# Kernel tuning notes

Measured on AMD Instinct MI355X. Metric: run time of the kernel, lower is better.

Reference implementation:

```python
import jax, jax.numpy as jnp
import numpy as np

N = 100000  # number of nodes
E = 3200000  # number of edges (avg degree 32)


def spmm(rows, cols, vals, Y):
    # sparse A (COO) @ dense Y : gather rows of Y at cols, scale, scatter-add to rows
    return jax.ops.segment_sum(vals[:, None] * Y[cols], rows, num_segments=N)


def setup_inputs() -> dict:
    key = jax.random.key(0)
    kx, kr, kc, kv, k0, k1 = jax.random.split(key, 6)
    X = jax.random.normal(kx, (N, 512), dtype=jnp.float32)
    edge_rows = jax.random.randint(kr, (E,), 0, N, dtype=jnp.int32)
    edge_cols = jax.random.randint(kc, (E,), 0, N, dtype=jnp.int32)
    edge_vals = jax.random.uniform(kv, (E,), dtype=jnp.float32)
    W0 = jax.random.normal(k0, (512, 256), dtype=jnp.float32) * 0.05
    W1 = jax.random.normal(k1, (256, 64), dtype=jnp.float32) * 0.05
    return {"X": X, "edge_rows": edge_rows, "edge_cols": edge_cols,
            "edge_vals": edge_vals, "W0": W0, "W1": W1}


def reference(X, edge_rows, edge_cols, edge_vals, W0, W1):
    # layer 1: A_hat @ (X W0), relu
    H1 = jax.nn.relu(spmm(edge_rows, edge_cols, edge_vals, X @ W0))  # [N, H]
    # layer 2: A_hat @ (H1 W1), softmax over classes
    Z = spmm(edge_rows, edge_cols, edge_vals, H1 @ W1)  # [N, F]
    return jax.nn.softmax(Z, axis=-1)
```

## Files before the change

### kernel.cpp

```cpp
#include <hip/hip_runtime.h>
#include <hip/hip_bf16.h>
#include <hip/hip_fp16.h>
#include <cstdint>

#define N_NODES 100000
#define N_EDGES 3200000
#define F_IN    512
#define F_HID   256
#define F_OUT   64
#define CAP     96

typedef _Float16 half8_t __attribute__((ext_vector_type(8)));
typedef _Float16 half4_t __attribute__((ext_vector_type(4)));
typedef float    float4_t __attribute__((ext_vector_type(4)));


__global__ __launch_bounds__(256) void zero_cursors_kernel(int* __restrict__ cursor, int n) {
    int i = blockIdx.x * 256 + threadIdx.x;
    if (i < n) cursor[i] = 0;
}

__global__ __launch_bounds__(256) void ell_scatter_kernel(
    const int* __restrict__ rows, const int* __restrict__ cols,
    const float* __restrict__ vals, int* __restrict__ cursor,
    int* __restrict__ ell_col, float* __restrict__ ell_val, int e_count) {
    int e = blockIdx.x * 256 + threadIdx.x;
    if (e >= e_count) return;
    int r = rows[e];
    int p = atomicAdd(&cursor[r], 1);
    if (p < CAP) {
        ell_col[(size_t)r * CAP + p] = cols[e];
        ell_val[(size_t)r * CAP + p] = vals[e];
    }
}


__global__ __launch_bounds__(256) void convert_w_kernel(
    const float* __restrict__ W0, const float* __restrict__ W1,
    _Float16* __restrict__ W0T, _Float16* __restrict__ W1T) {
    int i = blockIdx.x * 256 + threadIdx.x;
    if (i < F_HID * F_IN) {
        int n = i >> 9, k = i & 511;
        W0T[i] = (_Float16)W0[k * F_HID + n];
    }
    int j = i - F_HID * F_IN;
    if (j >= 0 && j < F_OUT * F_HID) {
        int n = j >> 8, k = j & 255;
        W1T[j] = (_Float16)W1[k * F_OUT + n];
    }
}


__global__ __launch_bounds__(256) void gemm1_mfma_kernel(
    const float* __restrict__ X, const _Float16* __restrict__ W0T,
    _Float16* __restrict__ H0) {
    const int wave = threadIdx.x >> 6;
    const int lane = threadIdx.x & 63;
    const int l15  = lane & 15;
    const int quad = lane >> 4;
    const int m0   = blockIdx.x * 64;
    const int n0   = wave * 64;

    float4_t acc[4][4] = {};

    int row[4];
    #pragma unroll
    for (int mt = 0; mt < 4; mt++) {
        int r = m0 + mt * 16 + l15;
        row[mt] = r < N_NODES ? r : N_NODES - 1;
    }

    for (int k0 = 0; k0 < F_IN; k0 += 32) {
        const int kk = k0 + quad * 8;
        half8_t b[4];
        #pragma unroll
        for (int nt = 0; nt < 4; nt++)
            b[nt] = *(const half8_t*)(W0T + (size_t)(n0 + nt * 16 + l15) * F_IN + kk);

        half8_t a[4];
        #pragma unroll
        for (int mt = 0; mt < 4; mt++) {
            const float* p = X + (size_t)row[mt] * F_IN + kk;
            float4_t lo = *(const float4_t*)p;
            float4_t hi = *(const float4_t*)(p + 4);
            half8_t f;
            f[0] = (_Float16)lo[0]; f[1] = (_Float16)lo[1];
            f[2] = (_Float16)lo[2]; f[3] = (_Float16)lo[3];
            f[4] = (_Float16)hi[0]; f[5] = (_Float16)hi[1];
            f[6] = (_Float16)hi[2]; f[7] = (_Float16)hi[3];
            a[mt] = f;
        }

        #pragma unroll
        for (int mt = 0; mt < 4; mt++)
            #pragma unroll
            for (int nt = 0; nt < 4; nt++)
                acc[mt][nt] = __builtin_amdgcn_mfma_f32_16x16x32_f16(
                    a[mt], b[nt], acc[mt][nt], 0, 0, 0);
    }

    #pragma unroll
    for (int mt = 0; mt < 4; mt++)
        #pragma unroll
        for (int reg = 0; reg < 4; reg++) {
            int m = m0 + mt * 16 + quad * 4 + reg;
            if (m < N_NODES) {
                #pragma unroll
                for (int nt = 0; nt < 4; nt++)
                    H0[(size_t)m * F_HID + n0 + nt * 16 + l15] =
                        (_Float16)acc[mt][nt][reg];
            }
        }
}


__global__ __launch_bounds__(256) void gemm2_mfma_kernel(
    const _Float16* __restrict__ H1, const _Float16* __restrict__ W1T,
    _Float16* __restrict__ H2) {
    const int wave = threadIdx.x >> 6;
    const int lane = threadIdx.x & 63;
    const int l15  = lane & 15;
    const int quad = lane >> 4;
    const int m0   = blockIdx.x * 64 + wave * 16;

    int r = m0 + l15;
    if (r >= N_NODES) r = N_NODES - 1;

    float4_t acc[4] = {};

    for (int k0 = 0; k0 < F_HID; k0 += 32) {
        const int kk = k0 + quad * 8;
        half8_t a = *(const half8_t*)(H1 + (size_t)r * F_HID + kk);
        #pragma unroll
        for (int nt = 0; nt < 4; nt++) {
            half8_t b = *(const half8_t*)(W1T + (size_t)(nt * 16 + l15) * F_HID + kk);
            acc[nt] = __builtin_amdgcn_mfma_f32_16x16x32_f16(a, b, acc[nt], 0, 0, 0);
        }
    }

    #pragma unroll
    for (int reg = 0; reg < 4; reg++) {
        int m = m0 + quad * 4 + reg;
        if (m < N_NODES) {
            #pragma unroll
            for (int nt = 0; nt < 4; nt++)
                H2[(size_t)m * F_OUT + nt * 16 + l15] = (_Float16)acc[nt][reg];
        }
    }
}


__global__ __launch_bounds__(256) void spmm_relu_kernel(
    const _Float16* __restrict__ H0, const int* __restrict__ ell_col,
    const float* __restrict__ ell_val, const int* __restrict__ cursor,
    _Float16* __restrict__ H1) {
    const int r = blockIdx.x * 4 + (threadIdx.x >> 6);
    const int t = threadIdx.x & 63;
    int n = cursor[r]; if (n > CAP) n = CAP;
    const int*   cols = ell_col + (size_t)r * CAP;
    const float* vals = ell_val + (size_t)r * CAP;
    const half4_t* H0v = (const half4_t*)H0;

    float4_t acc = {};
    int j = 0;
    for (; j + 4 <= n; j += 4) {
        int4   c = *(const int4*)(cols + j);
        float4 v = *(const float4*)(vals + j);
        half4_t g0 = H0v[(size_t)c.x * 64 + t];
        half4_t g1 = H0v[(size_t)c.y * 64 + t];
        half4_t g2 = H0v[(size_t)c.z * 64 + t];
        half4_t g3 = H0v[(size_t)c.w * 64 + t];
        #pragma unroll
        for (int i = 0; i < 4; i++) {
            acc[i] = fmaf(v.x, (float)g0[i], acc[i]);
            acc[i] = fmaf(v.y, (float)g1[i], acc[i]);
            acc[i] = fmaf(v.z, (float)g2[i], acc[i]);
            acc[i] = fmaf(v.w, (float)g3[i], acc[i]);
        }
    }
    for (; j < n; j++) {
        half4_t g = H0v[(size_t)cols[j] * 64 + t];
        float vv = vals[j];
        #pragma unroll
        for (int i = 0; i < 4; i++) acc[i] = fmaf(vv, (float)g[i], acc[i]);
    }
    half4_t o;
    #pragma unroll
    for (int i = 0; i < 4; i++) o[i] = (_Float16)fmaxf(acc[i], 0.f);
    ((half4_t*)H1)[(size_t)r * 64 + t] = o;
}


__global__ __launch_bounds__(256) void spmm_softmax_kernel(
    const _Float16* __restrict__ H2, const int* __restrict__ ell_col,
    const float* __restrict__ ell_val, const int* __restrict__ cursor,
    float* __restrict__ out) {
    const int lane = threadIdx.x & 63;
    const int r = blockIdx.x * 4 + (threadIdx.x >> 6);
    int n = cursor[r]; if (n > CAP) n = CAP;
    const int*   cols = ell_col + (size_t)r * CAP;
    const float* vals = ell_val + (size_t)r * CAP;
    float acc = 0.f;
    int j = 0;
    for (; j + 4 <= n; j += 4) {
        int4   c = *(const int4*)(cols + j);
        float4 v = *(const float4*)(vals + j);
        acc = fmaf(v.x, (float)H2[(size_t)c.x * F_OUT + lane], acc);
        acc = fmaf(v.y, (float)H2[(size_t)c.y * F_OUT + lane], acc);
        acc = fmaf(v.z, (float)H2[(size_t)c.z * F_OUT + lane], acc);
        acc = fmaf(v.w, (float)H2[(size_t)c.w * F_OUT + lane], acc);
    }
    for (; j < n; j++)
        acc = fmaf(vals[j], (float)H2[(size_t)cols[j] * F_OUT + lane], acc);

    float m = acc;
    #pragma unroll
    for (int o = 32; o >= 1; o >>= 1) m = fmaxf(m, __shfl_xor(m, o, 64));
    float e = expf(acc - m);
    float s = e;
    #pragma unroll
    for (int o = 32; o >= 1; o >>= 1) s += __shfl_xor(s, o, 64);
    out[(size_t)r * F_OUT + lane] = e / s;
}


extern "C" void kernel_launch(void* const* d_in, const int* in_sizes, int n_in,
                              void* d_out, int out_size, void* d_ws, size_t ws_size,
                              hipStream_t stream) {
    const float* X     = (const float*)d_in[0];
    const int*   erows = (const int*)  d_in[1];
    const int*   ecols = (const int*)  d_in[2];
    const float* evals = (const float*)d_in[3];
    const float* W0    = (const float*)d_in[4];
    const float* W1    = (const float*)d_in[5];
    float* out = (float*)d_out;

    char* p = (char*)d_ws;
    _Float16* H0  = (_Float16*)p; p += (size_t)N_NODES * F_HID * 2;
    _Float16* H1  = (_Float16*)p; p += (size_t)N_NODES * F_HID * 2;
    _Float16* H2  = (_Float16*)p; p += (size_t)N_NODES * F_OUT * 2;
    _Float16* W0T = (_Float16*)p; p += (size_t)F_HID * F_IN * 2;
    _Float16* W1T = (_Float16*)p; p += (size_t)F_OUT * F_HID * 2;
    int*   cursor  = (int*)p;     p += (size_t)N_NODES * 4;
    int*   ell_col = (int*)p;     p += (size_t)N_NODES * CAP * 4;
    float* ell_val = (float*)p;

    zero_cursors_kernel<<<(N_NODES + 255) / 256, 256, 0, stream>>>(cursor, N_NODES);
    ell_scatter_kernel<<<(N_EDGES + 255) / 256, 256, 0, stream>>>(
        erows, ecols, evals, cursor, ell_col, ell_val, N_EDGES);
    convert_w_kernel<<<(F_HID * F_IN + F_OUT * F_HID + 255) / 256, 256, 0, stream>>>(
        W0, W1, W0T, W1T);

    gemm1_mfma_kernel<<<(N_NODES + 63) / 64, 256, 0, stream>>>(X, W0T, H0);

    spmm_relu_kernel<<<N_NODES / 4, 256, 0, stream>>>(H0, ell_col, ell_val, cursor, H1);

    gemm2_mfma_kernel<<<(N_NODES + 63) / 64, 256, 0, stream>>>(H1, W1T, H2);

    spmm_softmax_kernel<<<N_NODES / 4, 256, 0, stream>>>(H2, ell_col, ell_val, cursor, out);
}
```

Baseline: 989.7 us.

## Interleave ELL col/val, pad cursors, retile GEMM1, widen SpMM gathers

Packs ELL column and value into one uint2 array so each edge is a single 8-byte load. Pads the per-row atomic cursors to a 16-int stride to spread atomic contention. GEMM1 uses a pre-swizzled W0 fragment layout and a 2x2 wave tiling (32 rows by 128 columns per wave), so the X rows each wave reloads and converts are halved and B loads are contiguous. Both SpMM kernels now split each wave into two half-waves that process alternate edges with wider 16-byte or 4-byte gathers, then combine via a shuffle. The padded cursor array adds zeroing traffic and the per-wave GEMM1 B loads double.

```diff
diff --git a/kernel.cpp b/kernel.cpp
--- a/kernel.cpp
+++ b/kernel.cpp
@@ -9,9 +9,10 @@
 #define F_HID   256
 #define F_OUT   64
 #define CAP     96
-
-typedef _Float16 half8_t __attribute__((ext_vector_type(8)));
-typedef _Float16 half4_t __attribute__((ext_vector_type(4)));
+#define CSTRIDE 16
+
+typedef _Float16 half8_t  __attribute__((ext_vector_type(8)));
+typedef _Float16 half2_t  __attribute__((ext_vector_type(2)));
 typedef float    float4_t __attribute__((ext_vector_type(4)));
 
 
@@ -23,25 +24,30 @@
 __global__ __launch_bounds__(256) void ell_scatter_kernel(
     const int* __restrict__ rows, const int* __restrict__ cols,
     const float* __restrict__ vals, int* __restrict__ cursor,
-    int* __restrict__ ell_col, float* __restrict__ ell_val, int e_count) {
+    uint2* __restrict__ ell, int e_count) {
     int e = blockIdx.x * 256 + threadIdx.x;
     if (e >= e_count) return;
     int r = rows[e];
-    int p = atomicAdd(&cursor[r], 1);
+    int p = atomicAdd(&cursor[r * CSTRIDE], 1);
     if (p < CAP) {
-        ell_col[(size_t)r * CAP + p] = cols[e];
-        ell_val[(size_t)r * CAP + p] = vals[e];
+        ell[(size_t)r * CAP + p] = make_uint2((unsigned)cols[e], __float_as_uint(vals[e]));
     }
 }
 
 
 __global__ __launch_bounds__(256) void convert_w_kernel(
     const float* __restrict__ W0, const float* __restrict__ W1,
-    _Float16* __restrict__ W0T, _Float16* __restrict__ W1T) {
+    _Float16* __restrict__ W0F, _Float16* __restrict__ W1T) {
     int i = blockIdx.x * 256 + threadIdx.x;
     if (i < F_HID * F_IN) {
-        int n = i >> 9, k = i & 511;
-        W0T[i] = (_Float16)W0[k * F_HID + n];
+        int j    = i & 7;
+        int nt   = (i >> 3) & 15;
+        int l15  = (i >> 7) & 15;
+        int quad = (i >> 11) & 3;
+        int ks   = i >> 13;
+        int n = nt * 16 + l15;
+        int k = ks * 32 + quad * 8 + j;
+        W0F[i] = (_Float16)W0[k * F_HID + n];
     }
     int j = i - F_HID * F_IN;
     if (j >= 0 && j < F_OUT * F_HID) {
@@ -52,34 +58,31 @@
 
 
 __global__ __launch_bounds__(256) void gemm1_mfma_kernel(
-    const float* __restrict__ X, const _Float16* __restrict__ W0T,
+    const float* __restrict__ X, const _Float16* __restrict__ W0F,
     _Float16* __restrict__ H0) {
     const int wave = threadIdx.x >> 6;
     const int lane = threadIdx.x & 63;
     const int l15  = lane & 15;
     const int quad = lane >> 4;
-    const int m0   = blockIdx.x * 64;
-    const int n0   = wave * 64;
-
-    float4_t acc[4][4] = {};
-
-    int row[4];
-    #pragma unroll
-    for (int mt = 0; mt < 4; mt++) {
+    const int rowhalf = wave & 1;
+    const int colhalf = wave >> 1;
+    const int m0 = blockIdx.x * 64 + rowhalf * 32;
+
+    float4_t acc[2][8] = {};
+
+    int row[2];
+    #pragma unroll
+    for (int mt = 0; mt < 2; mt++) {
         int r = m0 + mt * 16 + l15;
         row[mt] = r < N_NODES ? r : N_NODES - 1;
     }
 
-    for (int k0 = 0; k0 < F_IN; k0 += 32) {
-        const int kk = k0 + quad * 8;
-        half8_t b[4];
-        #pragma unroll
-        for (int nt = 0; nt < 4; nt++)
-            b[nt] = *(const half8_t*)(W0T + (size_t)(n0 + nt * 16 + l15) * F_IN + kk);
-
-        half8_t a[4];
-        #pragma unroll
-        for (int mt = 0; mt < 4; mt++) {
+    for (int ks = 0; ks < 16; ks++) {
+        const int kk = ks * 32 + quad * 8;
+
+        half8_t a[2];
+        #pragma unroll
+        for (int mt = 0; mt < 2; mt++) {
             const float* p = X + (size_t)row[mt] * F_IN + kk;
             float4_t lo = *(const float4_t*)p;
             float4_t hi = *(const float4_t*)(p + 4);
@@ -91,24 +94,30 @@
             a[mt] = f;
         }
 
-        #pragma unroll
-        for (int mt = 0; mt < 4; mt++)
+        const _Float16* bp = W0F + ((((size_t)ks * 4 + quad) * 16 + l15) * 128 + colhalf * 64);
+        half8_t b[8];
+        #pragma unroll
+        for (int ntl = 0; ntl < 8; ntl++)
+            b[ntl] = *(const half8_t*)(bp + ntl * 8);
+
+        #pragma unroll
+        for (int mt = 0; mt < 2; mt++)
             #pragma unroll
-            for (int nt = 0; nt < 4; nt++)
-                acc[mt][nt] = __builtin_amdgcn_mfma_f32_16x16x32_f16(
-                    a[mt], b[nt], acc[mt][nt], 0, 0, 0);
-    }
-
-    #pragma unroll
-    for (int mt = 0; mt < 4; mt++)
+            for (int ntl = 0; ntl < 8; ntl++)
+                acc[mt][ntl] = __builtin_amdgcn_mfma_f32_16x16x32_f16(
+                    a[mt], b[ntl], acc[mt][ntl], 0, 0, 0);
+    }
+
+    #pragma unroll
+    for (int mt = 0; mt < 2; mt++)
         #pragma unroll
         for (int reg = 0; reg < 4; reg++) {
             int m = m0 + mt * 16 + quad * 4 + reg;
             if (m < N_NODES) {
                 #pragma unroll
-                for (int nt = 0; nt < 4; nt++)
-                    H0[(size_t)m * F_HID + n0 + nt * 16 + l15] =
-                        (_Float16)acc[mt][nt][reg];
+                for (int ntl = 0; ntl < 8; ntl++)
+                    H0[(size_t)m * F_HID + colhalf * 128 + ntl * 16 + l15] =
+                        (_Float16)acc[mt][ntl][reg];
             }
         }
 }
@@ -151,76 +160,121 @@
 
 
 __global__ __launch_bounds__(256) void spmm_relu_kernel(
-    const _Float16* __restrict__ H0, const int* __restrict__ ell_col,
-    const float* __restrict__ ell_val, const int* __restrict__ cursor,
-    _Float16* __restrict__ H1) {
-    const int r = blockIdx.x * 4 + (threadIdx.x >> 6);
-    const int t = threadIdx.x & 63;
-    int n = cursor[r]; if (n > CAP) n = CAP;
-    const int*   cols = ell_col + (size_t)r * CAP;
-    const float* vals = ell_val + (size_t)r * CAP;
-    const half4_t* H0v = (const half4_t*)H0;
-
-    float4_t acc = {};
+    const _Float16* __restrict__ H0, const uint2* __restrict__ ell,
+    const int* __restrict__ cursor, _Float16* __restrict__ H1) {
+    const int r    = blockIdx.x * 4 + (threadIdx.x >> 6);
+    const int lane = threadIdx.x & 63;
+    const int sub  = lane >> 5;
+    const int f8   = lane & 31;
+    int n = cursor[r * CSTRIDE]; if (n > CAP) n = CAP;
+    const uint2* pr = ell + (size_t)r * CAP;
+    const half8_t* H0v = (const half8_t*)H0;
+
+    float acc[8] = {};
     int j = 0;
-    for (; j + 4 <= n; j += 4) {
-        int4   c = *(const int4*)(cols + j);
-        float4 v = *(const float4*)(vals + j);
-        half4_t g0 = H0v[(size_t)c.x * 64 + t];
-        half4_t g1 = H0v[(size_t)c.y * 64 + t];
-        half4_t g2 = H0v[(size_t)c.z * 64 + t];
-        half4_t g3 = H0v[(size_t)c.w * 64 + t];
-        #pragma unroll
-        for (int i = 0; i < 4; i++) {
-            acc[i] = fmaf(v.x, (float)g0[i], acc[i]);
-            acc[i] = fmaf(v.y, (float)g1[i], acc[i]);
-            acc[i] = fmaf(v.z, (float)g2[i], acc[i]);
-            acc[i] = fmaf(v.w, (float)g3[i], acc[i]);
-        }
-    }
-    for (; j < n; j++) {
-        half4_t g = H0v[(size_t)cols[j] * 64 + t];
-        float vv = vals[j];
-        #pragma unroll
-        for (int i = 0; i < 4; i++) acc[i] = fmaf(vv, (float)g[i], acc[i]);
-    }
-    half4_t o;
-    #pragma unroll
-    for (int i = 0; i < 4; i++) o[i] = (_Float16)fmaxf(acc[i], 0.f);
-    ((half4_t*)H1)[(size_t)r * 64 + t] = o;
+    for (; j + 8 <= n; j += 8) {
+        uint2 p0 = pr[j     + sub];
+        uint2 p1 = pr[j + 2 + sub];
+        uint2 p2 = pr[j + 4 + sub];
+        uint2 p3 = pr[j + 6 + sub];
+        half8_t g0 = H0v[(size_t)(int)p0.x * 32 + f8];
+        half8_t g1 = H0v[(size_t)(int)p1.x * 32 + f8];
+        half8_t g2 = H0v[(size_t)(int)p2.x * 32 + f8];
+        half8_t g3 = H0v[(size_t)(int)p3.x * 32 + f8];
+        float v0 = __uint_as_float(p0.y);
+        float v1 = __uint_as_float(p1.y);
+        float v2 = __uint_as_float(p2.y);
+        float v3 = __uint_as_float(p3.y);
+        #pragma unroll
+        for (int i = 0; i < 8; i++) {
+            acc[i] = fmaf(v0, (float)g0[i], acc[i]);
+            acc[i] = fmaf(v1, (float)g1[i], acc[i]);
+            acc[i] = fmaf(v2, (float)g2[i], acc[i]);
+            acc[i] = fmaf(v3, (float)g3[i], acc[i]);
+        }
+    }
+    for (; j + 2 <= n; j += 2) {
+        uint2 p = pr[j + sub];
+        half8_t g = H0v[(size_t)(int)p.x * 32 + f8];
+        float v = __uint_as_float(p.y);
+        #pragma unroll
+        for (int i = 0; i < 8; i++) acc[i] = fmaf(v, (float)g[i], acc[i]);
+    }
+    if (j < n && sub == 0) {
+        uint2 p = pr[j];
+        half8_t g = H0v[(size_t)(int)p.x * 32 + f8];
+        float v = __uint_as_float(p.y);
+        #pragma unroll
+        for (int i = 0; i < 8; i++) acc[i] = fmaf(v, (float)g[i], acc[i]);
+    }
+    #pragma unroll
+    for (int i = 0; i < 8; i++) acc[i] += __shfl_xor(acc[i], 32, 64);
+    if (sub == 0) {
+        half8_t o;
+        #pragma unroll
+        for (int i = 0; i < 8; i++) o[i] = (_Float16)fmaxf(acc[i], 0.f);
+        ((half8_t*)H1)[(size_t)r * 32 + f8] = o;
+    }
 }
 
 
 __global__ __launch_bounds__(256) void spmm_softmax_kernel(
-    const _Float16* __restrict__ H2, const int* __restrict__ ell_col,
-    const float* __restrict__ ell_val, const int* __restrict__ cursor,
-    float* __restrict__ out) {
+    const _Float16* __restrict__ H2, const uint2* __restrict__ ell,
+    const int* __restrict__ cursor, float* __restrict__ out) {
+    const int r    = blockIdx.x * 4 + (threadIdx.x >> 6);
     const int lane = threadIdx.x & 63;
-    const int r = blockIdx.x * 4 + (threadIdx.x >> 6);
-    int n = cursor[r]; if (n > CAP) n = CAP;
-    const int*   cols = ell_col + (size_t)r * CAP;
-    const float* vals = ell_val + (size_t)r * CAP;
-    float acc = 0.f;
+    const int sub  = lane >> 5;
+    const int c2   = lane & 31;
+    int n = cursor[r * CSTRIDE]; if (n > CAP) n = CAP;
+    const uint2* pr = ell + (size_t)r * CAP;
+    const half2_t* H2v = (const half2_t*)H2;
+
+    float a0 = 0.f, a1 = 0.f;
     int j = 0;
-    for (; j + 4 <= n; j += 4) {
-        int4   c = *(const int4*)(cols + j);
-        float4 v = *(const float4*)(vals + j);
-        acc = fmaf(v.x, (float)H2[(size_t)c.x * F_OUT + lane], acc);
-        acc = fmaf(v.y, (float)H2[(size_t)c.y * F_OUT + lane], acc);
-        acc = fmaf(v.z, (float)H2[(size_t)c.z * F_OUT + lane], acc);
-        acc = fmaf(v.w, (float)H2[(size_t)c.w * F_OUT + lane], acc);
-    }
-    for (; j < n; j++)
-        acc = fmaf(vals[j], (float)H2[(size_t)cols[j] * F_OUT + lane], acc);
-
-    float m = acc;
-    #pragma unroll
-    for (int o = 32; o >= 1; o >>= 1) m = fmaxf(m, __shfl_xor(m, o, 64));
-    float e = expf(acc - m);
-    float s = e;
-    #pragma unroll
-    for (int o = 32; o >= 1; o >>= 1) s += __shfl_xor(s, o, 64);
-    out[(size_t)r * F_OUT + lane] = e / s;
+    for (; j + 8 <= n; j += 8) {
+        uint2 p0 = pr[j     + sub];
+        uint2 p1 = pr[j + 2 + sub];
+        uint2 p2 = pr[j + 4 + sub];
+        uint2 p3 = pr[j + 6 + sub];
+        half2_t g0 = H2v[(size_t)(int)p0.x * 32 + c2];
+        half2_t g1 = H2v[(size_t)(int)p1.x * 32 + c2];
+        half2_t g2 = H2v[(size_t)(int)p2.x * 32 + c2];
+        half2_t g3 = H2v[(size_t)(int)p3.x * 32 + c2];
+        float v0 = __uint_as_float(p0.y);
+        float v1 = __uint_as_float(p1.y);
+        float v2 = __uint_as_float(p2.y);
+        float v3 = __uint_as_float(p3.y);
+        a0 = fmaf(v0, (float)g0[0], a0); a1 = fmaf(v0, (float)g0[1], a1);
+        a0 = fmaf(v1, (float)g1[0], a0); a1 = fmaf(v1, (float)g1[1], a1);
+        a0 = fmaf(v2, (float)g2[0], a0); a1 = fmaf(v2, (float)g2[1], a1);
+        a0 = fmaf(v3, (float)g3[0], a0); a1 = fmaf(v3, (float)g3[1], a1);
+    }
+    for (; j + 2 <= n; j += 2) {
+        uint2 p = pr[j + sub];
+        half2_t g = H2v[(size_t)(int)p.x * 32 + c2];
+        float v = __uint_as_float(p.y);
+        a0 = fmaf(v, (float)g[0], a0); a1 = fmaf(v, (float)g[1], a1);
+    }
+    if (j < n && sub == 0) {
+        uint2 p = pr[j];
+        half2_t g = H2v[(size_t)(int)p.x * 32 + c2];
+        float v = __uint_as_float(p.y);
+        a0 = fmaf(v, (float)g[0], a0); a1 = fmaf(v, (float)g[1], a1);
+    }
+    a0 += __shfl_xor(a0, 32, 64);
+    a1 += __shfl_xor(a1, 32, 64);
+
+    float m = fmaxf(a0, a1);
+    #pragma unroll
+    for (int o = 16; o >= 1; o >>= 1) m = fmaxf(m, __shfl_xor(m, o, 64));
+    float e0 = expf(a0 - m), e1 = expf(a1 - m);
+    float s = e0 + e1;
+    #pragma unroll
+    for (int o = 16; o >= 1; o >>= 1) s += __shfl_xor(s, o, 64);
+    if (sub == 0) {
+        float2 o2 = make_float2(e0 / s, e1 / s);
+        ((float2*)out)[(size_t)r * 32 + c2] = o2;
+    }
 }
 
 
@@ -239,23 +293,23 @@
     _Float16* H0  = (_Float16*)p; p += (size_t)N_NODES * F_HID * 2;
     _Float16* H1  = (_Float16*)p; p += (size_t)N_NODES * F_HID * 2;
     _Float16* H2  = (_Float16*)p; p += (size_t)N_NODES * F_OUT * 2;
-    _Float16* W0T = (_Float16*)p; p += (size_t)F_HID * F_IN * 2;
+    _Float16* W0F = (_Float16*)p; p += (size_t)F_HID * F_IN * 2;
     _Float16* W1T = (_Float16*)p; p += (size_t)F_OUT * F_HID * 2;
-    int*   cursor  = (int*)p;     p += (size_t)N_NODES * 4;
-    int*   ell_col = (int*)p;     p += (size_t)N_NODES * CAP * 4;
-    float* ell_val = (float*)p;
-
-    zero_cursors_kernel<<<(N_NODES + 255) / 256, 256, 0, stream>>>(cursor, N_NODES);
+    int*   cursor = (int*)p;      p += (size_t)N_NODES * CSTRIDE * 4;
+    uint2* ell    = (uint2*)p;
+
+    zero_cursors_kernel<<<(N_NODES * CSTRIDE + 255) / 256, 256, 0, stream>>>(
+        cursor, N_NODES * CSTRIDE);
     ell_scatter_kernel<<<(N_EDGES + 255) / 256, 256, 0, stream>>>(
-        erows, ecols, evals, cursor, ell_col, ell_val, N_EDGES);
+        erows, ecols, evals, cursor, ell, N_EDGES);
     convert_w_kernel<<<(F_HID * F_IN + F_OUT * F_HID + 255) / 256, 256, 0, stream>>>(
-        W0, W1, W0T, W1T);
-
-    gemm1_mfma_kernel<<<(N_NODES + 63) / 64, 256, 0, stream>>>(X, W0T, H0);
-
-    spmm_relu_kernel<<<N_NODES / 4, 256, 0, stream>>>(H0, ell_col, ell_val, cursor, H1);
+        W0, W1, W0F, W1T);
+
+    gemm1_mfma_kernel<<<(N_NODES + 63) / 64, 256, 0, stream>>>(X, W0F, H0);
+
+    spmm_relu_kernel<<<N_NODES / 4, 256, 0, stream>>>(H0, ell, cursor, H1);
 
     gemm2_mfma_kernel<<<(N_NODES + 63) / 64, 256, 0, stream>>>(H1, W1T, H2);
 
-    spmm_softmax_kernel<<<N_NODES / 4, 256, 0, stream>>>(H2, ell_col, ell_val, cursor, out);
-}
+    spmm_softmax_kernel<<<N_NODES / 4, 256, 0, stream>>>(H2, ell, cursor, out);
+}
```

Measured after the change: 1.019 ms. 1.03x slower.
